# Optimization experiments

Measured on AMD Instinct MI355X. Metric: run time of the kernel, lower is better.

## Reference

```python
import jax, jax.numpy as jnp
import numpy as np

S, I, H, C, B = 512, 1, 256, 10, 2048

def _xavier(key, shape):
    fan_out, fan_in = shape
    std = (2.0 / (fan_in + fan_out)) ** 0.5
    return jax.random.normal(key, shape, dtype=jnp.float32) * std

def setup_inputs() -> dict:
    key = jax.random.key(0)
    k_x, k_hx, k_hh, k_ph = jax.random.split(key, 4)
    return {
        "x": jax.random.normal(k_x, (B, S), dtype=jnp.float32),
        "W_hx": _xavier(k_hx, (H, I)),
        "W_hh": _xavier(k_hh, (H, H)),
        "W_ph": _xavier(k_ph, (C, H)),
        "b_h": jnp.zeros((H, 1), dtype=jnp.float32),
        "b_p": jnp.zeros((C, 1), dtype=jnp.float32),
    }

def reference(x, W_hx, W_hh, W_ph, b_h, b_p):
    # x: [B, S]; hidden state h: [H, B]
    batch = x.shape[0]
    h0 = jnp.zeros((W_hh.shape[0], batch), dtype=x.dtype)
    xs = x.T  # [S, B], one row per timestep

    def step(h, x_t):
        # x_t: [B] -> [1, B]; W_hx: [H, 1]
        h_new = jnp.tanh(W_hx @ x_t[None, :] + W_hh @ h + b_h)
        return h_new, None

    h_final, _ = jax.lax.scan(step, h0, xs)
    # output: [B, C]
    return (W_ph @ h_final + b_p).T
```

## Files before the change

kernel.cpp:

```cpp
#include <hip/hip_runtime.h>


#define SEQ    512
#define HID    256
#define NCLS   10
#define BN     16
#define NT     512
#define XP     17

typedef _Float16 f16x8 __attribute__((ext_vector_type(8)));
typedef _Float16 f16x4 __attribute__((ext_vector_type(4)));
typedef float    f32x4 __attribute__((ext_vector_type(4)));

__global__ __launch_bounds__(NT)
__attribute__((amdgpu_waves_per_eu(2, 2)))
void rnn_mfma(
    const float* __restrict__ x,
    const float* __restrict__ W_hx,
    const float* __restrict__ W_hh,
    const float* __restrict__ W_ph,
    const float* __restrict__ b_h,
    const float* __restrict__ b_p,
    float* __restrict__ out)
{
    __shared__ __align__(16) _Float16 hT[2][BN][HID];
    __shared__ __align__(16) float xs[SEQ + 2][XP];

    const int tid  = threadIdx.x;
    const int lane = tid & 63;
    const int wave = tid >> 6;
    const int n16  = lane & 15;
    const int quad = lane >> 4;
    const int sw   = (n16 & 7) ^ ((n16 >> 3) << 2);
    const int b0   = blockIdx.x * BN;

    const float SC = 2.885390081777926814f;

    f16x8 afrag[2][8];
#pragma unroll
    for (int mt = 0; mt < 2; ++mt) {
        const int row = wave * 32 + mt * 16 + n16;
#pragma unroll
        for (int ks = 0; ks < 8; ++ks) {
            const float4* p = (const float4*)&W_hh[row * HID + ks * 32 + quad * 8];
            float4 u = p[0], v = p[1];
            f16x8 a;
            a[0] = (_Float16)(SC * u.x); a[1] = (_Float16)(SC * u.y);
            a[2] = (_Float16)(SC * u.z); a[3] = (_Float16)(SC * u.w);
            a[4] = (_Float16)(SC * v.x); a[5] = (_Float16)(SC * v.y);
            a[6] = (_Float16)(SC * v.z); a[7] = (_Float16)(SC * v.w);
            afrag[mt][ks] = a;
        }
    }
    f32x4 bias[2], wxv[2];
#pragma unroll
    for (int mt = 0; mt < 2; ++mt)
#pragma unroll
        for (int r = 0; r < 4; ++r) {
            const int row = wave * 32 + mt * 16 + quad * 4 + r;
            bias[mt][r] = SC * b_h[row];
            wxv[mt][r]  = SC * W_hx[row];
        }

    int roff[8], woff[2];
#pragma unroll
    for (int ks = 0; ks < 8; ++ks)
        roff[ks] = (n16 * HID + (((4 * ks + quad) ^ sw) << 3)) * 2;
#pragma unroll
    for (int mt = 0; mt < 2; ++mt)
        woff[mt] = (n16 * HID +
                    (((4 * wave + 2 * mt + (quad >> 1)) ^ sw) << 3) +
                    (quad & 1) * 4) * 2;

    for (int i = tid; i < BN * SEQ / 4; i += NT) {
        const int n = i >> 7, t4 = (i & 127) * 4;
        float4 v = *(const float4*)&x[(b0 + n) * SEQ + t4];
        xs[t4 + 0][n] = v.x; xs[t4 + 1][n] = v.y;
        xs[t4 + 2][n] = v.z; xs[t4 + 3][n] = v.w;
    }
    for (int i = tid; i < BN * HID / 2; i += NT) ((float*)hT[0])[i] = 0.0f;
    __syncthreads();

    float xv = xs[0][n16];

#define RNN_STEP(T, RD, WR)                                                   \
    {                                                                         \
        const float xnxt = xs[(T) + 1][n16];      \
        const char* hb = (const char*)hT[RD];                                 \
        f16x8 bfr[8];                                                         \
        _Pragma("unroll")                                                     \
        for (int ks = 0; ks < 8; ++ks)                                        \
            bfr[ks] = *(const f16x8*)(hb + roff[ks]);                         \
        f32x4 acc0[2], acc1[2];                                               \
        _Pragma("unroll")                                                     \
        for (int mt = 0; mt < 2; ++mt) {                                      \
            f32x4 c0, c1;                                                     \
            _Pragma("unroll")                                                 \
            for (int r = 0; r < 4; ++r) {                                     \
                c0[r] = bias[mt][r];                                          \
                c1[r] = wxv[mt][r] * xv;                                      \
            }                                                                 \
            acc0[mt] = __builtin_amdgcn_mfma_f32_16x16x32_f16(                \
                afrag[mt][0], bfr[0], c0, 0, 0, 0);                           \
            acc1[mt] = __builtin_amdgcn_mfma_f32_16x16x32_f16(                \
                afrag[mt][1], bfr[1], c1, 0, 0, 0);                           \
        }                                                                     \
        _Pragma("unroll")                                                     \
        for (int ks = 2; ks < 8; ks += 2)                                     \
            _Pragma("unroll")                                                 \
            for (int mt = 0; mt < 2; ++mt) {                                  \
                acc0[mt] = __builtin_amdgcn_mfma_f32_16x16x32_f16(            \
                    afrag[mt][ks], bfr[ks], acc0[mt], 0, 0, 0);               \
                acc1[mt] = __builtin_amdgcn_mfma_f32_16x16x32_f16(            \
                    afrag[mt][ks + 1], bfr[ks + 1], acc1[mt], 0, 0, 0);       \
            }                                                                 \
        char* wb = (char*)hT[WR];                                             \
        _Pragma("unroll")                                                     \
        for (int mt = 0; mt < 2; ++mt) {                                      \
            f16x4 h4;                                                         \
            _Pragma("unroll")                                                 \
            for (int r = 0; r < 4; ++r) {                                     \
                float s  = acc0[mt][r] + acc1[mt][r];                         \
                float ex = __builtin_amdgcn_exp2f(s);                         \
                float rc = __builtin_amdgcn_rcpf(ex + 1.0f);                  \
                h4[r] = (_Float16)(1.0f - 2.0f * rc);                         \
            }                                                                 \
            *(f16x4*)(wb + woff[mt]) = h4;                                    \
        }                                                                     \
        xv = xnxt;                                                            \
        __syncthreads();                                                      \
    }

    for (int t = 0; t < SEQ; t += 2) {
        RNN_STEP(t, 0, 1);
        RNN_STEP(t + 1, 1, 0);
    }
#undef RNN_STEP

    if (tid < BN * NCLS) {
        const int b = tid / NCLS, c = tid % NCLS;
        const int sb = (b & 7) ^ ((b >> 3) << 2);
        float sum = b_p[c];
        const _Float16* hp = hT[0][b];
        for (int j = 0; j < HID; ++j) {
            const int ph = ((((j >> 3) ^ sb) << 3) | (j & 7));
            sum += W_ph[c * HID + j] * (float)hp[ph];
        }
        out[(b0 + b) * NCLS + c] = sum;
    }
}

extern "C" void kernel_launch(void* const* d_in, const int* in_sizes, int n_in,
                              void* d_out, int out_size, void* d_ws, size_t ws_size,
                              hipStream_t stream) {
    const float* x    = (const float*)d_in[0];
    const float* W_hx = (const float*)d_in[1];
    const float* W_hh = (const float*)d_in[2];
    const float* W_ph = (const float*)d_in[3];
    const float* b_h  = (const float*)d_in[4];
    const float* b_p  = (const float*)d_in[5];
    float* out = (float*)d_out;

    rnn_mfma<<<dim3(2048 / BN), dim3(NT), 0, stream>>>(
        x, W_hx, W_hh, W_ph, b_h, b_p, out);
}
```

Before: 353.7 us.

## Split hidden rows into two halves and software-pipeline the recurrence across a mid-step barrier

Hidden rows are remapped so each wave's first tile covers rows 0-127 and its second tile covers rows 128-255. Each step computes and writes the first half, hits a barrier, then loads the first-half columns of the new state for the next step while computing the second half from the old state. The aim is to hide LDS read latency of the next step behind the current step's MFMA work. In exchange the kernel takes two barriers per step, and each tile now runs as one serial 8-deep MFMA accumulation chain instead of interleaved independent accumulators, which lengthens dependent latency.

```diff
diff --git a/kernel.cpp b/kernel.cpp
--- a/kernel.cpp
+++ b/kernel.cpp
@@ -11,6 +11,8 @@
 typedef _Float16 f16x8 __attribute__((ext_vector_type(8)));
 typedef _Float16 f16x4 __attribute__((ext_vector_type(4)));
 typedef float    f32x4 __attribute__((ext_vector_type(4)));
+
+#define MFMA16(a, b, c) __builtin_amdgcn_mfma_f32_16x16x32_f16(a, b, c, 0, 0, 0)
 
 __global__ __launch_bounds__(NT)
 __attribute__((amdgpu_waves_per_eu(2, 2)))
@@ -39,7 +41,7 @@
     f16x8 afrag[2][8];
 #pragma unroll
     for (int mt = 0; mt < 2; ++mt) {
-        const int row = wave * 32 + mt * 16 + n16;
+        const int row = (wave + 8 * mt) * 16 + n16;
 #pragma unroll
         for (int ks = 0; ks < 8; ++ks) {
             const float4* p = (const float4*)&W_hh[row * HID + ks * 32 + quad * 8];
@@ -57,7 +59,7 @@
     for (int mt = 0; mt < 2; ++mt)
 #pragma unroll
         for (int r = 0; r < 4; ++r) {
-            const int row = wave * 32 + mt * 16 + quad * 4 + r;
+            const int row = (wave + 8 * mt) * 16 + quad * 4 + r;
             bias[mt][r] = SC * b_h[row];
             wxv[mt][r]  = SC * W_hx[row];
         }
@@ -69,7 +71,7 @@
 #pragma unroll
     for (int mt = 0; mt < 2; ++mt)
         woff[mt] = (n16 * HID +
-                    (((4 * wave + 2 * mt + (quad >> 1)) ^ sw) << 3) +
+                    (((2 * (wave + 8 * mt) + (quad >> 1)) ^ sw) << 3) +
                     (quad & 1) * 4) * 2;
 
     for (int i = tid; i < BN * SEQ / 4; i += NT) {
@@ -83,59 +85,75 @@
 
     float xv = xs[0][n16];
 
-#define RNN_STEP(T, RD, WR)                                                   \
+    f16x8 bA[4], bB[4];
+#pragma unroll
+    for (int k = 0; k < 4; ++k)
+        bA[k] = *(const f16x8*)((const char*)hT[0] + roff[k]);
+
+#define TANH_WRITE(ACC, MT)                                                   \
     {                                                                         \
-        const float xnxt = xs[(T) + 1][n16];      \
-        const char* hb = (const char*)hT[RD];                                 \
-        f16x8 bfr[8];                                                         \
+        f16x4 h4;                                                             \
         _Pragma("unroll")                                                     \
-        for (int ks = 0; ks < 8; ++ks)                                        \
-            bfr[ks] = *(const f16x8*)(hb + roff[ks]);                         \
-        f32x4 acc0[2], acc1[2];                                               \
+        for (int r = 0; r < 4; ++r) {                                         \
+            float ex = __builtin_amdgcn_exp2f(ACC[r]);                        \
+            float rc = __builtin_amdgcn_rcpf(ex + 1.0f);                      \
+            h4[r] = (_Float16)(1.0f - 2.0f * rc);                             \
+        }                                                                     \
+        *(f16x4*)(wb + woff[MT]) = h4;                                        \
+    }
+
+#define RNN_STEP(T, RD, WR, LI, LO)                                           \
+    {                                                                         \
+        const float xnxt = xs[(T) + 1][n16];                                  \
+        const char* rb = (const char*)hT[RD];                                 \
+        char*       wb = (char*)hT[WR];                                       \
+           \
+        f16x8 hi0 = *(const f16x8*)(rb + roff[4]);                            \
+        f16x8 hi1 = *(const f16x8*)(rb + roff[5]);                            \
+        f16x8 hi2 = *(const f16x8*)(rb + roff[6]);                            \
+        f16x8 hi3 = *(const f16x8*)(rb + roff[7]);                            \
+        f32x4 acc;                                                            \
         _Pragma("unroll")                                                     \
-        for (int mt = 0; mt < 2; ++mt) {                                      \
-            f32x4 c0, c1;                                                     \
-            _Pragma("unroll")                                                 \
-            for (int r = 0; r < 4; ++r) {                                     \
-                c0[r] = bias[mt][r];                                          \
-                c1[r] = wxv[mt][r] * xv;                                      \
-            }                                                                 \
-            acc0[mt] = __builtin_amdgcn_mfma_f32_16x16x32_f16(                \
-                afrag[mt][0], bfr[0], c0, 0, 0, 0);                           \
-            acc1[mt] = __builtin_amdgcn_mfma_f32_16x16x32_f16(                \
-                afrag[mt][1], bfr[1], c1, 0, 0, 0);                           \
-        }                                                                     \
+        for (int r = 0; r < 4; ++r)                                           \
+            acc[r] = fmaf(wxv[0][r], xv, bias[0][r]);                         \
+        acc = MFMA16(afrag[0][0], LI[0], acc);                                \
+        acc = MFMA16(afrag[0][1], LI[1], acc);                                \
+        acc = MFMA16(afrag[0][2], LI[2], acc);                                \
+        acc = MFMA16(afrag[0][3], LI[3], acc);                                \
+        acc = MFMA16(afrag[0][4], hi0, acc);                                  \
+        acc = MFMA16(afrag[0][5], hi1, acc);                                  \
+        acc = MFMA16(afrag[0][6], hi2, acc);                                  \
+        acc = MFMA16(afrag[0][7], hi3, acc);                                  \
+        TANH_WRITE(acc, 0)                                                    \
+        __syncthreads();              \
+               \
+        LO[0] = *(const f16x8*)((const char*)hT[WR] + roff[0]);               \
+        LO[1] = *(const f16x8*)((const char*)hT[WR] + roff[1]);               \
+        LO[2] = *(const f16x8*)((const char*)hT[WR] + roff[2]);               \
+        LO[3] = *(const f16x8*)((const char*)hT[WR] + roff[3]);               \
+        f32x4 acd;                                                            \
         _Pragma("unroll")                                                     \
-        for (int ks = 2; ks < 8; ks += 2)                                     \
-            _Pragma("unroll")                                                 \
-            for (int mt = 0; mt < 2; ++mt) {                                  \
-                acc0[mt] = __builtin_amdgcn_mfma_f32_16x16x32_f16(            \
-                    afrag[mt][ks], bfr[ks], acc0[mt], 0, 0, 0);               \
-                acc1[mt] = __builtin_amdgcn_mfma_f32_16x16x32_f16(            \
-                    afrag[mt][ks + 1], bfr[ks + 1], acc1[mt], 0, 0, 0);       \
-            }                                                                 \
-        char* wb = (char*)hT[WR];                                             \
-        _Pragma("unroll")                                                     \
-        for (int mt = 0; mt < 2; ++mt) {                                      \
-            f16x4 h4;                                                         \
-            _Pragma("unroll")                                                 \
-            for (int r = 0; r < 4; ++r) {                                     \
-                float s  = acc0[mt][r] + acc1[mt][r];                         \
-                float ex = __builtin_amdgcn_exp2f(s);                         \
-                float rc = __builtin_amdgcn_rcpf(ex + 1.0f);                  \
-                h4[r] = (_Float16)(1.0f - 2.0f * rc);                         \
-            }                                                                 \
-            *(f16x4*)(wb + woff[mt]) = h4;                                    \
-        }                                                                     \
+        for (int r = 0; r < 4; ++r)                                           \
+            acd[r] = fmaf(wxv[1][r], xv, bias[1][r]);                         \
+        acd = MFMA16(afrag[1][0], LI[0], acd);                                \
+        acd = MFMA16(afrag[1][1], LI[1], acd);                                \
+        acd = MFMA16(afrag[1][2], LI[2], acd);                                \
+        acd = MFMA16(afrag[1][3], LI[3], acd);                                \
+        acd = MFMA16(afrag[1][4], hi0, acd);                                  \
+        acd = MFMA16(afrag[1][5], hi1, acd);                                  \
+        acd = MFMA16(afrag[1][6], hi2, acd);                                  \
+        acd = MFMA16(afrag[1][7], hi3, acd);                                  \
+        TANH_WRITE(acd, 1)                                                    \
         xv = xnxt;                                                            \
-        __syncthreads();                                                      \
+        __syncthreads();              \
     }
 
     for (int t = 0; t < SEQ; t += 2) {
-        RNN_STEP(t, 0, 1);
-        RNN_STEP(t + 1, 1, 0);
+        RNN_STEP(t,     0, 1, bA, bB);
+        RNN_STEP(t + 1, 1, 0, bB, bA);
     }
 #undef RNN_STEP
+#undef TANH_WRITE
 
     if (tid < BN * NCLS) {
         const int b = tid / NCLS, c = tid % NCLS;
```

Measured after the change: 370.0 us. 1.05x slower.

## Ping-pong two batch groups per block, overlapping MFMA with tanh writeback

Applied to the files above, without the earlier changes.

Each block now handles 32 batch columns split into two 16-column groups of four waves. Each wave owns 64 hidden rows, holding 4x8 A fragments in registers. The groups alternate phases so one group's MFMA reads overlap the other group's tanh and h writeback, with each group keeping a single in-place h buffer. This halves the grid to 64 blocks and doubles the per-wave register footprint. It also adds two barriers per timestep, aiming to hide the transcendental and LDS write latency on the serial recurrence path.

```diff
diff --git a/kernel.cpp b/kernel.cpp
--- a/kernel.cpp
+++ b/kernel.cpp
@@ -4,13 +4,15 @@
 #define SEQ    512
 #define HID    256
 #define NCLS   10
-#define BN     16
+#define BN     32
 #define NT     512
-#define XP     17
+#define XP     33
 
 typedef _Float16 f16x8 __attribute__((ext_vector_type(8)));
 typedef _Float16 f16x4 __attribute__((ext_vector_type(4)));
 typedef float    f32x4 __attribute__((ext_vector_type(4)));
+
+#define MFMA16(a, b, c) __builtin_amdgcn_mfma_f32_16x16x32_f16(a, b, c, 0, 0, 0)
 
 __global__ __launch_bounds__(NT)
 __attribute__((amdgpu_waves_per_eu(2, 2)))
@@ -23,23 +25,26 @@
     const float* __restrict__ b_p,
     float* __restrict__ out)
 {
-    __shared__ __align__(16) _Float16 hT[2][BN][HID];
+    __shared__ __align__(16) _Float16 hT[2][16][HID];
     __shared__ __align__(16) float xs[SEQ + 2][XP];
 
     const int tid  = threadIdx.x;
     const int lane = tid & 63;
     const int wave = tid >> 6;
+    const int g    = wave >> 2;
+    const int w4   = wave & 3;
     const int n16  = lane & 15;
     const int quad = lane >> 4;
     const int sw   = (n16 & 7) ^ ((n16 >> 3) << 2);
+    const int col  = g * 16 + n16;
     const int b0   = blockIdx.x * BN;
 
     const float SC = 2.885390081777926814f;
 
-    f16x8 afrag[2][8];
+    f16x8 afrag[4][8];
 #pragma unroll
-    for (int mt = 0; mt < 2; ++mt) {
-        const int row = wave * 32 + mt * 16 + n16;
+    for (int i = 0; i < 4; ++i) {
+        const int row = w4 * 64 + i * 16 + n16;
 #pragma unroll
         for (int ks = 0; ks < 8; ++ks) {
             const float4* p = (const float4*)&W_hh[row * HID + ks * 32 + quad * 8];
@@ -49,28 +54,29 @@
             a[2] = (_Float16)(SC * u.z); a[3] = (_Float16)(SC * u.w);
             a[4] = (_Float16)(SC * v.x); a[5] = (_Float16)(SC * v.y);
             a[6] = (_Float16)(SC * v.z); a[7] = (_Float16)(SC * v.w);
-            afrag[mt][ks] = a;
+            afrag[i][ks] = a;
         }
     }
-    f32x4 bias[2], wxv[2];
+    f32x4 bias[4], wxv[4];
 #pragma unroll
-    for (int mt = 0; mt < 2; ++mt)
+    for (int i = 0; i < 4; ++i)
 #pragma unroll
         for (int r = 0; r < 4; ++r) {
-            const int row = wave * 32 + mt * 16 + quad * 4 + r;
-            bias[mt][r] = SC * b_h[row];
-            wxv[mt][r]  = SC * W_hx[row];
+            const int row = w4 * 64 + i * 16 + quad * 4 + r;
+            bias[i][r] = SC * b_h[row];
+            wxv[i][r]  = SC * W_hx[row];
         }
 
-    int roff[8], woff[2];
+    const char* hb = (const char*)hT[g];
+    int roff[8], woff[4];
 #pragma unroll
     for (int ks = 0; ks < 8; ++ks)
         roff[ks] = (n16 * HID + (((4 * ks + quad) ^ sw) << 3)) * 2;
 #pragma unroll
-    for (int mt = 0; mt < 2; ++mt)
-        woff[mt] = (n16 * HID +
-                    (((4 * wave + 2 * mt + (quad >> 1)) ^ sw) << 3) +
-                    (quad & 1) * 4) * 2;
+    for (int i = 0; i < 4; ++i)
+        woff[i] = (n16 * HID +
+                   (((2 * (w4 * 4 + i) + (quad >> 1)) ^ sw) << 3) +
+                   (quad & 1) * 4) * 2;
 
     for (int i = tid; i < BN * SEQ / 4; i += NT) {
         const int n = i >> 7, t4 = (i & 127) * 4;
@@ -78,70 +84,76 @@
         xs[t4 + 0][n] = v.x; xs[t4 + 1][n] = v.y;
         xs[t4 + 2][n] = v.z; xs[t4 + 3][n] = v.w;
     }
-    for (int i = tid; i < BN * HID / 2; i += NT) ((float*)hT[0])[i] = 0.0f;
+    for (int i = tid; i < 2 * 16 * HID / 2; i += NT) ((float*)hT)[i] = 0.0f;
     __syncthreads();
 
-    float xv = xs[0][n16];
+    float xv = xs[0][col];
+    f32x4 acc[4];
 
-#define RNN_STEP(T, RD, WR)                                                   \
+#define READ_MFMA(T)                                                          \
     {                                                                         \
-        const float xnxt = xs[(T) + 1][n16];      \
-        const char* hb = (const char*)hT[RD];                                 \
+        const float xnxt = xs[(T) + 1][col];                                  \
         f16x8 bfr[8];                                                         \
         _Pragma("unroll")                                                     \
         for (int ks = 0; ks < 8; ++ks)                                        \
             bfr[ks] = *(const f16x8*)(hb + roff[ks]);                         \
-        f32x4 acc0[2], acc1[2];                                               \
         _Pragma("unroll")                                                     \
-        for (int mt = 0; mt < 2; ++mt) {                                      \
-            f32x4 c0, c1;                                                     \
+        for (int i = 0; i < 4; ++i) {                                         \
+            f32x4 c0;                                                         \
             _Pragma("unroll")                                                 \
-            for (int r = 0; r < 4; ++r) {                                     \
-                c0[r] = bias[mt][r];                                          \
-                c1[r] = wxv[mt][r] * xv;                                      \
-            }                                                                 \
-            acc0[mt] = __builtin_amdgcn_mfma_f32_16x16x32_f16(                \
-                afrag[mt][0], bfr[0], c0, 0, 0, 0);                           \
-            acc1[mt] = __builtin_amdgcn_mfma_f32_16x16x32_f16(                \
-                afrag[mt][1], bfr[1], c1, 0, 0, 0);                           \
+            for (int r = 0; r < 4; ++r)                                       \
+                c0[r] = fmaf(wxv[i][r], xv, bias[i][r]);                      \
+            acc[i] = MFMA16(afrag[i][0], bfr[0], c0);                         \
         }                                                                     \
         _Pragma("unroll")                                                     \
-        for (int ks = 2; ks < 8; ks += 2)                                     \
+        for (int ks = 1; ks < 8; ++ks)                                        \
             _Pragma("unroll")                                                 \
-            for (int mt = 0; mt < 2; ++mt) {                                  \
-                acc0[mt] = __builtin_amdgcn_mfma_f32_16x16x32_f16(            \
-                    afrag[mt][ks], bfr[ks], acc0[mt], 0, 0, 0);               \
-                acc1[mt] = __builtin_amdgcn_mfma_f32_16x16x32_f16(            \
-                    afrag[mt][ks + 1], bfr[ks + 1], acc1[mt], 0, 0, 0);       \
-            }                                                                 \
-        char* wb = (char*)hT[WR];                                             \
+            for (int i = 0; i < 4; ++i)                                       \
+                acc[i] = MFMA16(afrag[i][ks], bfr[ks], acc[i]);               \
+        xv = xnxt;                                                            \
+    }
+
+#define TANH_WRITE()                                                          \
+    {                                                                         \
         _Pragma("unroll")                                                     \
-        for (int mt = 0; mt < 2; ++mt) {                                      \
+        for (int i = 0; i < 4; ++i) {                                         \
             f16x4 h4;                                                         \
             _Pragma("unroll")                                                 \
             for (int r = 0; r < 4; ++r) {                                     \
-                float s  = acc0[mt][r] + acc1[mt][r];                         \
-                float ex = __builtin_amdgcn_exp2f(s);                         \
+                float ex = __builtin_amdgcn_exp2f(acc[i][r]);                 \
                 float rc = __builtin_amdgcn_rcpf(ex + 1.0f);                  \
                 h4[r] = (_Float16)(1.0f - 2.0f * rc);                         \
             }                                                                 \
-            *(f16x4*)(wb + woff[mt]) = h4;                                    \
+            *(f16x4*)((char*)hb + woff[i]) = h4;                              \
         }                                                                     \
-        xv = xnxt;                                                            \
-        __syncthreads();                                                      \
     }
 
-    for (int t = 0; t < SEQ; t += 2) {
-        RNN_STEP(t, 0, 1);
-        RNN_STEP(t + 1, 1, 0);
+    for (int t = 0; t < SEQ; ++t) {
+        if (g == 0) {
+            READ_MFMA(t)
+        } else if (t > 0) {
+            TANH_WRITE()
+        }
+        __syncthreads();
+        if (g == 0) {
+            TANH_WRITE()
+        } else {
+            READ_MFMA(t)
+        }
+        __syncthreads();
     }
-#undef RNN_STEP
+    if (g == 1) { TANH_WRITE() }
+    __syncthreads();
+
+#undef READ_MFMA
+#undef TANH_WRITE
 
     if (tid < BN * NCLS) {
         const int b = tid / NCLS, c = tid % NCLS;
-        const int sb = (b & 7) ^ ((b >> 3) << 2);
+        const int bc = b & 15;
+        const int sb = (bc & 7) ^ ((bc >> 3) << 2);
         float sum = b_p[c];
-        const _Float16* hp = hT[0][b];
+        const _Float16* hp = hT[b >> 4][bc];
         for (int j = 0; j < HID; ++j) {
             const int ph = ((((j >> 3) ^ sb) << 3) | (j & 7));
             sum += W_ph[c * HID + j] * (float)hp[ph];
```

Result: slower. 582.0 us (+64.5%).

## Process two 16-column batch groups per block to halve grid and overlap tanh with MFMA

Applied to the files above, without the earlier changes.

Doubles the batch tile per workgroup from 16 to 32 columns, so each wave reuses its register-resident W_hh fragments for two MFMA column groups per timestep. The second group's MFMA chain is interleaved with the first group's tanh and store, hiding transcendental latency behind matrix work. This halves the number of blocks, fewer than the CU count so some CUs sit idle, and doubles the per-step serial work in each block. It also drops the split-accumulator chain and folds the x term into the bias with fma. Shared memory grows and the final output swizzle is adjusted for 32 rows.

```diff
diff --git a/kernel.cpp b/kernel.cpp
--- a/kernel.cpp
+++ b/kernel.cpp
@@ -4,13 +4,16 @@
 #define SEQ    512
 #define HID    256
 #define NCLS   10
-#define BN     16
+#define BN     32
 #define NT     512
-#define XP     17
+#define XP     33
+#define G1OFF  8192
 
 typedef _Float16 f16x8 __attribute__((ext_vector_type(8)));
 typedef _Float16 f16x4 __attribute__((ext_vector_type(4)));
 typedef float    f32x4 __attribute__((ext_vector_type(4)));
+
+#define MFMA16(a, b, c) __builtin_amdgcn_mfma_f32_16x16x32_f16(a, b, c, 0, 0, 0)
 
 __global__ __launch_bounds__(NT)
 __attribute__((amdgpu_waves_per_eu(2, 2)))
@@ -81,53 +84,66 @@
     for (int i = tid; i < BN * HID / 2; i += NT) ((float*)hT[0])[i] = 0.0f;
     __syncthreads();
 
-    float xv = xs[0][n16];
+    float xv0 = xs[0][n16];
+    float xv1 = xs[0][16 + n16];
+
+#define TANH_W(ACC, MT, GOFF)                                                 \
+    {                                                                         \
+        f16x4 h4;                                                             \
+        _Pragma("unroll")                                                     \
+        for (int r = 0; r < 4; ++r) {                                         \
+            float ex = __builtin_amdgcn_exp2f(ACC[r]);                        \
+            float rc = __builtin_amdgcn_rcpf(ex + 1.0f);                      \
+            h4[r] = (_Float16)(1.0f - 2.0f * rc);                             \
+        }                                                                     \
+        *(f16x4*)(wb + woff[MT] + (GOFF)) = h4;                               \
+    }
 
 #define RNN_STEP(T, RD, WR)                                                   \
     {                                                                         \
-        const float xnxt = xs[(T) + 1][n16];      \
-        const char* hb = (const char*)hT[RD];                                 \
-        f16x8 bfr[8];                                                         \
+        const float xn0 = xs[(T) + 1][n16];                                   \
+        const float xn1 = xs[(T) + 1][16 + n16];                              \
+        const char* rb = (const char*)hT[RD];                                 \
+        char*       wb = (char*)hT[WR];                                       \
+        f16x8 bfr0[8], bfr1[8];                                               \
         _Pragma("unroll")                                                     \
         for (int ks = 0; ks < 8; ++ks)                                        \
-            bfr[ks] = *(const f16x8*)(hb + roff[ks]);                         \
-        f32x4 acc0[2], acc1[2];                                               \
+            bfr0[ks] = *(const f16x8*)(rb + roff[ks]);                        \
+        _Pragma("unroll")                                                     \
+        for (int ks = 0; ks < 8; ++ks)                                        \
+            bfr1[ks] = *(const f16x8*)(rb + roff[ks] + G1OFF);                \
+        f32x4 a0[2], a1[2];                                                   \
         _Pragma("unroll")                                                     \
         for (int mt = 0; mt < 2; ++mt) {                                      \
-            f32x4 c0, c1;                                                     \
+            f32x4 c0;                                                         \
             _Pragma("unroll")                                                 \
-            for (int r = 0; r < 4; ++r) {                                     \
-                c0[r] = bias[mt][r];                                          \
-                c1[r] = wxv[mt][r] * xv;                                      \
-            }                                                                 \
-            acc0[mt] = __builtin_amdgcn_mfma_f32_16x16x32_f16(                \
-                afrag[mt][0], bfr[0], c0, 0, 0, 0);                           \
-            acc1[mt] = __builtin_amdgcn_mfma_f32_16x16x32_f16(                \
-                afrag[mt][1], bfr[1], c1, 0, 0, 0);                           \
+            for (int r = 0; r < 4; ++r)                                       \
+                c0[r] = fmaf(wxv[mt][r], xv0, bias[mt][r]);                   \
+            a0[mt] = MFMA16(afrag[mt][0], bfr0[0], c0);                       \
         }                                                                     \
         _Pragma("unroll")                                                     \
-        for (int ks = 2; ks < 8; ks += 2)                                     \
+        for (int ks = 1; ks < 8; ++ks)                                        \
             _Pragma("unroll")                                                 \
-            for (int mt = 0; mt < 2; ++mt) {                                  \
-                acc0[mt] = __builtin_amdgcn_mfma_f32_16x16x32_f16(            \
-                    afrag[mt][ks], bfr[ks], acc0[mt], 0, 0, 0);               \
-                acc1[mt] = __builtin_amdgcn_mfma_f32_16x16x32_f16(            \
-                    afrag[mt][ks + 1], bfr[ks + 1], acc1[mt], 0, 0, 0);       \
-            }                                                                 \
-        char* wb = (char*)hT[WR];                                             \
+            for (int mt = 0; mt < 2; ++mt)                                    \
+                a0[mt] = MFMA16(afrag[mt][ks], bfr0[ks], a0[mt]);             \
         _Pragma("unroll")                                                     \
         for (int mt = 0; mt < 2; ++mt) {                                      \
-            f16x4 h4;                                                         \
+            f32x4 c1;                                                         \
             _Pragma("unroll")                                                 \
-            for (int r = 0; r < 4; ++r) {                                     \
-                float s  = acc0[mt][r] + acc1[mt][r];                         \
-                float ex = __builtin_amdgcn_exp2f(s);                         \
-                float rc = __builtin_amdgcn_rcpf(ex + 1.0f);                  \
-                h4[r] = (_Float16)(1.0f - 2.0f * rc);                         \
-            }                                                                 \
-            *(f16x4*)(wb + woff[mt]) = h4;                                    \
+            for (int r = 0; r < 4; ++r)                                       \
+                c1[r] = fmaf(wxv[mt][r], xv1, bias[mt][r]);                   \
+            a1[mt] = MFMA16(afrag[mt][0], bfr1[0], c1);                       \
         }                                                                     \
-        xv = xnxt;                                                            \
+        TANH_W(a0[0], 0, 0)                                                   \
+        TANH_W(a0[1], 1, 0)                                                   \
+        _Pragma("unroll")                                                     \
+        for (int ks = 1; ks < 8; ++ks)                                        \
+            _Pragma("unroll")                                                 \
+            for (int mt = 0; mt < 2; ++mt)                                    \
+                a1[mt] = MFMA16(afrag[mt][ks], bfr1[ks], a1[mt]);             \
+        TANH_W(a1[0], 0, G1OFF)                                               \
+        TANH_W(a1[1], 1, G1OFF)                                               \
+        xv0 = xn0; xv1 = xn1;                                                 \
         __syncthreads();                                                      \
     }
 
@@ -136,10 +152,11 @@
         RNN_STEP(t + 1, 1, 0);
     }
 #undef RNN_STEP
+#undef TANH_W
 
     if (tid < BN * NCLS) {
         const int b = tid / NCLS, c = tid % NCLS;
-        const int sb = (b & 7) ^ ((b >> 3) << 2);
+        const int sb = (b & 7) ^ (((b >> 3) & 1) << 2);
         float sum = b_p[c];
         const _Float16* hp = hT[0][b];
         for (int j = 0; j < HID; ++j) {
```

Measured after the change: 556.3 us. +57.3%, slower.
